# Kernel optimization log

Hardware: AMD Instinct MI355X
Metric: run time of the kernel (lower is better)

Reference implementation:

```python
import jax, jax.numpy as jnp
import numpy as np

H = 16          # num_attention_heads
DH = 64         # attention_head_size = hidden // heads
WINDOW = 128    # window_size
GLOBAL_RATIO = 0.1
SCALE = 1.0 / np.sqrt(DH)


def _combined_mask(seq_len):
    # sliding window: |i-j| <= window_size // 2
    pos = jnp.arange(seq_len)
    dist = pos[None, :] - pos[:, None]
    window_mask = jnp.abs(dist) <= (WINDOW // 2)
    # global tokens: first max(1, int(S * ratio)) positions, full row+col
    num_global = max(1, int(seq_len * GLOBAL_RATIO))
    is_global = pos < num_global
    global_mask = is_global[:, None] | is_global[None, :]
    return window_mask | global_mask  # [S, S] bool


def setup_inputs() -> dict:
    key = jax.random.key(0)
    ks = jax.random.split(key, 9)
    B, S, Dm = 2, 2048, 1024
    s = 0.02
    return {
        "hidden_states": jax.random.normal(ks[0], (B, S, Dm), jnp.float32),
        "Wq": jax.random.normal(ks[1], (Dm, Dm), jnp.float32) * s,
        "bq": jax.random.normal(ks[2], (Dm,), jnp.float32) * s,
        "Wk": jax.random.normal(ks[3], (Dm, Dm), jnp.float32) * s,
        "bk": jax.random.normal(ks[4], (Dm,), jnp.float32) * s,
        "Wv": jax.random.normal(ks[5], (Dm, Dm), jnp.float32) * s,
        "bv": jax.random.normal(ks[6], (Dm,), jnp.float32) * s,
        "Wo": jax.random.normal(ks[7], (Dm, Dm), jnp.float32) * s,
        "bo": jax.random.normal(ks[8], (Dm,), jnp.float32) * s,
    }


def reference(hidden_states, Wq, bq, Wk, bk, Wv, bv, Wo, bo):
    B, S, Dm = hidden_states.shape

    def heads(x):  # [B,S,Dm] -> [B,H,S,Dh]
        return x.reshape(B, S, H, DH).transpose(0, 2, 1, 3)

    q = heads(hidden_states @ Wq.T + bq)
    k = heads(hidden_states @ Wk.T + bk)
    v = heads(hidden_states @ Wv.T + bv)

    scores = jnp.einsum("bhqd,bhkd->bhqk", q, k) * SCALE
    mask = _combined_mask(S)  # [S,S] bool, True = attend
    scores = scores + jnp.where(mask, 0.0, -10000.0)[None, None]

    probs = jax.nn.softmax(scores, axis=-1)
    ctx = jnp.einsum("bhqk,bhkd->bhqd", probs, v)
    ctx = ctx.transpose(0, 2, 1, 3).reshape(B, S, Dm)
    return ctx @ Wo.T + bo
```

## Files before the change

### kernel.cpp

```cpp
#include <hip/hip_runtime.h>


#define B_   2
#define S_   2048
#define DM   1024
#define H_   16
#define NG   204
#define BS_  4096
#define SCL2 0.1803368801111204f
#define NEGF -3.0e38f

typedef unsigned short u16;
typedef unsigned int   u32;
typedef __attribute__((ext_vector_type(8))) short frag8;
typedef __attribute__((ext_vector_type(4))) short frag4;
typedef __attribute__((ext_vector_type(4))) float f32x4;

#define MFMA16(A, Bf, C) __builtin_amdgcn_mfma_f32_16x16x32_bf16((A), (Bf), (C), 0, 0, 0)

__device__ __forceinline__ f32x4 mfma_16x16x16_bf16(frag4 a, frag4 b, f32x4 c) {
#if defined(__HIP_DEVICE_COMPILE__)
  return __builtin_amdgcn_mfma_f32_16x16x16bf16_1k(a, b, c, 0, 0, 0);
#else
  (void)a; (void)b;
  return c;
#endif
}

#define GLD16(g, l)                                                              \
  __builtin_amdgcn_global_load_lds((const __attribute__((address_space(1))) u32*)(g), \
                                   (__attribute__((address_space(3))) u32*)(l), 16, 0, 0)
#define EXP2(x) exp2f(x)

__device__ __forceinline__ u16 f2bf(float f) {
  union { float f; u32 u; } c; c.f = f;
  u32 u = c.u + 0x7fffu + ((c.u >> 16) & 1u);
  return (u16)(u >> 16);
}

#if defined(__HIP_DEVICE_COMPILE__)
__device__ __forceinline__ u32 cvtpk_bf16(float lo, float hi) {
  u32 r;
  asm("v_cvt_pk_bf16_f32 %0, %1, %2" : "=v"(r) : "v"(lo), "v"(hi));
  return r;
}
#else
__device__ __forceinline__ u32 cvtpk_bf16(float lo, float hi) { (void)lo; (void)hi; return 0; }
#endif

__device__ __forceinline__ frag4 pack4_bf16(float a, float b, float c, float d) {
  union { u32 u[2]; frag4 f; } x;
  x.u[0] = cvtpk_bf16(a, b);
  x.u[1] = cvtpk_bf16(c, d);
  return x.f;
}

__global__ void cvt_all(const float* __restrict__ X,  const float* __restrict__ Wq,
                        const float* __restrict__ Wk, const float* __restrict__ Wv,
                        const float* __restrict__ Wo,
                        u16* Xb, u16* Wqb, u16* Wkb, u16* Wvb, u16* Wob) {
  const int chunk = blockIdx.y;
  const float* src; u16* dst;
  if (chunk < 4)      { src = X + (size_t)chunk * 1048576; dst = Xb + (size_t)chunk * 1048576; }
  else if (chunk == 4){ src = Wq; dst = Wqb; }
  else if (chunk == 5){ src = Wk; dst = Wkb; }
  else if (chunk == 6){ src = Wv; dst = Wvb; }
  else                { src = Wo; dst = Wob; }
  int i = blockIdx.x * 256 + threadIdx.x;
  float4 v = ((const float4*)src)[i];
  u32 lo = (u32)f2bf(v.x) | ((u32)f2bf(v.y) << 16);
  u32 hi = (u32)f2bf(v.z) | ((u32)f2bf(v.w) << 16);
  ((uint2*)dst)[i] = make_uint2(lo, hi);
}

__device__ __forceinline__ void gemm_mainloop(const u16* __restrict__ A, const u16* __restrict__ Bm,
                                              int bm, int bn, u16* As, u16* Bs,
                                              f32x4 acc[4][4]) {
  const int tid = threadIdx.x;
  const int wv = tid >> 6, lane = tid & 63, l15 = lane & 15, quad = lane >> 4;
  const int wm = wv & 1, wn = wv >> 1;

  const u16* gA[4]; const u16* gB[4];
#pragma unroll
  for (int c = 0; c < 4; ++c) {
    int idx = (wv * 4 + c) * 64 + lane;
    int r = idx >> 3;
    int cb = (idx & 7) ^ (r & 7);
    gA[c] = A  + (size_t)(bm + r) * DM + cb * 8;
    gB[c] = Bm + (size_t)(bn + r) * DM + cb * 8;
  }

  int offA[4][2], offB[4][2];
#pragma unroll
  for (int i = 0; i < 4; ++i)
#pragma unroll
    for (int h = 0; h < 2; ++h) {
      int mA = wm * 64 + i * 16 + l15;
      int mB = wn * 64 + i * 16 + l15;
      int cb = (quad + h * 4) ^ (l15 & 7);
      offA[i][h] = ((mA << 3) + cb) << 4;
      offB[i][h] = ((mB << 3) + cb) << 4;
    }

  for (int k0 = 0; k0 < DM; k0 += 64) {
#pragma unroll
    for (int c = 0; c < 4; ++c) {
      GLD16(gA[c] + k0, (char*)As + (wv * 4 + c) * 1024);
      GLD16(gB[c] + k0, (char*)Bs + (wv * 4 + c) * 1024);
    }
    __syncthreads();
    frag8 af[4][2], bf[4][2];
#pragma unroll
    for (int i = 0; i < 4; ++i) {
      af[i][0] = *(const frag8*)((const char*)As + offA[i][0]);
      af[i][1] = *(const frag8*)((const char*)As + offA[i][1]);
      bf[i][0] = *(const frag8*)((const char*)Bs + offB[i][0]);
      bf[i][1] = *(const frag8*)((const char*)Bs + offB[i][1]);
    }
#pragma unroll
    for (int h = 0; h < 2; ++h)
#pragma unroll
      for (int i = 0; i < 4; ++i)
#pragma unroll
        for (int j = 0; j < 4; ++j)
          acc[i][j] = MFMA16(af[i][h], bf[j][h], acc[i][j]);
    __syncthreads();
  }
}

__global__ __launch_bounds__(256, 3) void gemm_qkv(const u16* __restrict__ Xb,
    const u16* __restrict__ Wqb, const u16* __restrict__ Wkb, const u16* __restrict__ Wvb,
    const float* __restrict__ bq, const float* __restrict__ bk, const float* __restrict__ bv,
    u16* __restrict__ Qb, u16* __restrict__ Kb, u16* __restrict__ Vt) {
  __shared__ u16 As[8192], Bs[8192];
  const int bm = blockIdx.y * 128;
  const int which = blockIdx.x >> 3;
  const int bnl = (blockIdx.x & 7) * 128;
  const u16* W = (which == 0) ? Wqb : (which == 1) ? Wkb : Wvb;
  const float* bias = (which == 0) ? bq : (which == 1) ? bk : bv;

  f32x4 acc[4][4] = {};
  gemm_mainloop(Xb, W, bm, bnl, As, Bs, acc);

  const int tid = threadIdx.x, wv = tid >> 6, lane = tid & 63, l15 = lane & 15, quad = lane >> 4;
  const int wm = wv & 1, wn = wv >> 1;
  if (which < 2) {
    u16* O = (which == 0) ? Qb : Kb;
    const float scl = (which == 0) ? SCL2 : 1.0f;
#pragma unroll
    for (int j = 0; j < 4; ++j) {
      int col = bnl + wn * 64 + j * 16 + l15;
      float bb = bias[col];
#pragma unroll
      for (int i = 0; i < 4; ++i) {
        int row0 = bm + wm * 64 + i * 16 + quad * 4;
#pragma unroll
        for (int r = 0; r < 4; ++r)
          O[(size_t)(row0 + r) * DM + col] = f2bf((acc[i][j][r] + bb) * scl);
      }
    }
  } else {
#pragma unroll
    for (int j = 0; j < 4; ++j) {
      int col = bnl + wn * 64 + j * 16 + l15;
      float bb = bias[col];
#pragma unroll
      for (int i = 0; i < 4; ++i) {
        int row0 = bm + wm * 64 + i * 16 + quad * 4;
        u32 lo = (u32)f2bf(acc[i][j][0] + bb) | ((u32)f2bf(acc[i][j][1] + bb) << 16);
        u32 hi = (u32)f2bf(acc[i][j][2] + bb) | ((u32)f2bf(acc[i][j][3] + bb) << 16);
        *(uint2*)&Vt[(size_t)col * BS_ + row0] = make_uint2(lo, hi);
      }
    }
  }
}

__global__ __launch_bounds__(256, 3) void gemm_wo(const u16* __restrict__ Cx,
    const u16* __restrict__ Wob, const float* __restrict__ bo, float* __restrict__ out) {
  __shared__ u16 As[8192], Bs[8192];
  const int bm = blockIdx.y * 128, bn = blockIdx.x * 128;

  f32x4 acc[4][4] = {};
  gemm_mainloop(Cx, Wob, bm, bn, As, Bs, acc);

  const int tid = threadIdx.x, wv = tid >> 6, lane = tid & 63, l15 = lane & 15, quad = lane >> 4;
  const int wm = wv & 1, wn = wv >> 1;
#pragma unroll
  for (int j = 0; j < 4; ++j) {
    int col = bn + wn * 64 + j * 16 + l15;
    float bb = bo[col];
#pragma unroll
    for (int i = 0; i < 4; ++i) {
      int row0 = bm + wm * 64 + i * 16 + quad * 4;
#pragma unroll
      for (int r = 0; r < 4; ++r)
        out[(size_t)(row0 + r) * DM + col] = acc[i][j][r] + bb;
    }
  }
}

__global__ __launch_bounds__(256, 3) void attn_kernel(const u16* __restrict__ Q,
                                                      const u16* __restrict__ K,
                                                      const u16* __restrict__ Vt,
                                                      u16* __restrict__ Ctx,
                                                      float* __restrict__ Op,
                                                      float* __restrict__ Lp) {
  __shared__ u16 Ks[2][4096];
  __shared__ u16 Vs[2][4096];

  const int tid = threadIdx.x, w = tid >> 6, lane = tid & 63, l15 = lane & 15, quad = lane >> 4;
  const int blk = blockIdx.x;
  const int bh = blk & 31, unit = blk >> 5;
  const int b = bh >> 4, h = bh & 15;
  const bool heavy = unit < 8;
  const int strip = heavy ? (unit >> 2) : 0;
  const int q0 = heavy ? strip * 128 : 256 + (unit - 8) * 128;
  const int qw = q0 + w * 16;

  frag8 bq[2][2];
#pragma unroll
  for (int g = 0; g < 2; ++g) {
    const u16* qrow = Q + (size_t)(b * S_ + qw + g * 64 + l15) * DM + h * 64;
    bq[g][0] = *(const frag8*)(qrow + quad * 8);
    bq[g][1] = *(const frag8*)(qrow + quad * 8 + 32);
  }

  const u16* gK[2]; const u16* gV[2]; int ldso[2];
#pragma unroll
  for (int c = 0; c < 2; ++c) {
    int sl = (w * 2 + c) * 64 + lane;
    int r = sl >> 3;
    int fr = (r & 7) ^ (((r >> 3) & 1) << 2);
    int cb = (sl & 7) ^ fr;
    gK[c] = K  + (size_t)(b * S_ + r) * DM + h * 64 + cb * 8;
    gV[c] = Vt + (size_t)(h * 64 + r) * BS_ + (size_t)b * S_ + cb * 8;
    ldso[c] = (w * 2 + c) * 1024;
  }

  const int fl = (l15 & 7) ^ (((l15 >> 3) & 1) << 2);
  int offKb[2];
#pragma unroll
  for (int hh = 0; hh < 2; ++hh)
    offKb[hh] = ((l15 << 3) + ((quad + hh * 4) ^ fl)) << 4;
  int offVb[4];
#pragma unroll
  for (int kg = 0; kg < 4; ++kg)
    offVb[kg] = ((((l15 << 3) + ((((kg << 1) | (quad >> 1))) ^ fl)) << 4)
                 | ((quad & 1) << 3));

  int mlo[2]; u32 mspan[2];
#pragma unroll
  for (int g = 0; g < 2; ++g) {
    int qi = qw + g * 64 + l15;
    bool qg = qi < NG;
    mlo[g]   = qg ? (int)0x80000000 : (qi - 64);
    mspan[g] = qg ? 0xFFFFFFFFu : 128u;
  }
  const frag4 ones = {(short)0x3F80, (short)0x3F80, (short)0x3F80, (short)0x3F80};

  f32x4 o[2][4] = {};
  f32x4 o_l[2] = {};

  auto stage = [&](int t, int buf) {
#pragma unroll
    for (int c = 0; c < 2; ++c) {
      GLD16(gK[c] + (size_t)t * 64 * DM, (char*)Ks[buf] + ldso[c]);
      GLD16(gV[c] + t * 64,              (char*)Vs[buf] + ldso[c]);
    }
  };

  auto step = [&](int kt, int p, int mmode) {
    int gok0 = 1, gok1 = 1;
    if (mmode == 1) {
      const int k0s = kt * 64;
      const int ql1 = qw + 64;
      gok0 = (qw  < NG) || ((k0s + 63 >= qw  - 64) && (k0s <= qw  + 79));
      gok1 = (ql1 < NG) || ((k0s + 63 >= ql1 - 64) && (k0s <= ql1 + 79));
      if (!(gok0 | gok1)) return;
    }
    const char* kb_ = (const char*)Ks[p];
    const char* vb_ = (const char*)Vs[p];
    frag8 ak[4][2];
#pragma unroll
    for (int kg = 0; kg < 4; ++kg) {
      ak[kg][0] = *(const frag8*)(kb_ + offKb[0] + kg * 2048);
      ak[kg][1] = *(const frag8*)(kb_ + offKb[1] + kg * 2048);
    }
    const int k0 = kt * 64;
    const int gok[2] = {gok0, gok1};
    frag4 pk[2][4];
#pragma unroll
    for (int g = 0; g < 2; ++g) {
      if (!gok[g]) continue;
      f32x4 st[4] = {};
#pragma unroll
      for (int kg = 0; kg < 4; ++kg) {
        st[kg] = MFMA16(ak[kg][0], bq[g][0], st[kg]);
        st[kg] = MFMA16(ak[kg][1], bq[g][1], st[kg]);
      }
      if (mmode) {
#pragma unroll
        for (int kg = 0; kg < 4; ++kg) {
          float pr[4];
#pragma unroll
          for (int r = 0; r < 4; ++r) {
            int kc = k0 + kg * 16 + quad * 4 + r;
            bool act = ((u32)(kc - mlo[g]) <= mspan[g]);
            if (mmode == 2) act = act || (kc < NG);
            float e = EXP2(st[kg][r]);
            pr[r] = act ? e : 0.0f;
          }
          pk[g][kg] = pack4_bf16(pr[0], pr[1], pr[2], pr[3]);
        }
      } else {
#pragma unroll
        for (int kg = 0; kg < 4; ++kg)
          pk[g][kg] = pack4_bf16(EXP2(st[kg][0]), EXP2(st[kg][1]),
                                 EXP2(st[kg][2]), EXP2(st[kg][3]));
      }
    }
    if (gok0 & gok1) {
#pragma unroll
      for (int kg = 0; kg < 4; ++kg) {
        o_l[0] = mfma_16x16x16_bf16(ones, pk[0][kg], o_l[0]);
        o_l[1] = mfma_16x16x16_bf16(ones, pk[1][kg], o_l[1]);
#pragma unroll
        for (int nt = 0; nt < 4; ++nt) {
          frag4 av = *(const frag4*)(vb_ + offVb[kg] + nt * 2048);
          o[0][nt] = mfma_16x16x16_bf16(av, pk[0][kg], o[0][nt]);
          o[1][nt] = mfma_16x16x16_bf16(av, pk[1][kg], o[1][nt]);
        }
      }
    } else if (gok0) {
#pragma unroll
      for (int kg = 0; kg < 4; ++kg) {
        o_l[0] = mfma_16x16x16_bf16(ones, pk[0][kg], o_l[0]);
#pragma unroll
        for (int nt = 0; nt < 4; ++nt) {
          frag4 av = *(const frag4*)(vb_ + offVb[kg] + nt * 2048);
          o[0][nt] = mfma_16x16x16_bf16(av, pk[0][kg], o[0][nt]);
        }
      }
    } else {
#pragma unroll
      for (int kg = 0; kg < 4; ++kg) {
        o_l[1] = mfma_16x16x16_bf16(ones, pk[1][kg], o_l[1]);
#pragma unroll
        for (int nt = 0; nt < 4; ++nt) {
          frag4 av = *(const frag4*)(vb_ + offVb[kg] + nt * 2048);
          o[1][nt] = mfma_16x16x16_bf16(av, pk[1][kg], o[1][nt]);
        }
      }
    }
  };

  if (heavy) {
    const int seg = unit & 3;
    const int kt0 = seg * 8;
    const bool dm = (strip == 1);
    int p = 0;
    stage(kt0, 0);
#pragma unroll 1
    for (int tt = 0; tt < 8; ++tt) {
      __syncthreads();
      if (tt < 7) stage(kt0 + tt + 1, p ^ 1);
      const int kt = kt0 + tt;
      const int mm = dm ? ((kt == 3) ? 2 : ((kt > 2) ? 1 : 0)) : 0;
      step(kt, p, mm);
      p ^= 1;
    }
    float* op = Op + ((size_t)((bh * 2 + strip) * 4 + seg)) * 8192;
    float* lp = Lp + ((size_t)((bh * 2 + strip) * 4 + seg)) * 128;
#pragma unroll
    for (int g = 0; g < 2; ++g) {
      int rl = g * 64 + w * 16 + l15;
      if (quad == 0) lp[rl] = o_l[g][0];
#pragma unroll
      for (int nt = 0; nt < 4; ++nt)
        *(float4*)&op[rl * 64 + nt * 16 + quad * 4] =
            make_float4(o[g][nt][0], o[g][nt][1], o[g][nt][2], o[g][nt][3]);
    }
    return;
  }

  auto activef = [&](int t) {
    int k0 = t * 64;
    return (k0 < NG) || (k0 + 63 >= q0 - 64 && k0 <= q0 + 127 + 64);
  };
  auto nextt = [&](int cur) { int n = cur + 1; while (n < 32 && !activef(n)) ++n; return n; };

  int kt = 0, p = 0;
  stage(0, 0);
  for (;;) {
    int ktn = nextt(kt);
    bool more = ktn < 32;
    __syncthreads();
    if (more) stage(ktn, p ^ 1);
    const int mm = (kt == 3) ? 2 : ((kt > 2) ? 1 : 0);
    step(kt, p, mm);
    if (!more) break;
    kt = ktn; p ^= 1;
  }

#pragma unroll
  for (int g = 0; g < 2; ++g) {
    float inv = 1.0f / o_l[g][0];
    u16* crow = Ctx + (size_t)((size_t)b * S_ + qw + g * 64 + l15) * DM + h * 64;
#pragma unroll
    for (int nt = 0; nt < 4; ++nt) {
      u32 lo = (u32)f2bf(o[g][nt][0] * inv) | ((u32)f2bf(o[g][nt][1] * inv) << 16);
      u32 hi = (u32)f2bf(o[g][nt][2] * inv) | ((u32)f2bf(o[g][nt][3] * inv) << 16);
      *(uint2*)&crow[nt * 16 + quad * 4] = make_uint2(lo, hi);
    }
  }
}

__global__ __launch_bounds__(256) void combine_kernel(const float* __restrict__ Op,
                                                      const float* __restrict__ Lp,
                                                      u16* __restrict__ Ctx) {
  const int blk = blockIdx.x;
  const int bh = blk & 31, s64 = blk >> 5;
  const int b = bh >> 4, h = bh & 15;
  const int t = threadIdx.x;
  const int row = t >> 2, colg = (t & 3) * 16;
  const int gq = s64 * 64 + row;
  const int strip = gq >> 7, rIn = gq & 127;

  const float* opb = Op + ((size_t)(bh * 2 + strip) * 4) * 8192;
  const float* lpb = Lp + ((size_t)(bh * 2 + strip) * 4) * 128;

  float l = lpb[rIn] + lpb[128 + rIn] + lpb[256 + rIn] + lpb[384 + rIn];
  float acc[16];
#pragma unroll
  for (int e = 0; e < 16; ++e) acc[e] = opb[rIn * 64 + colg + e];
#pragma unroll
  for (int seg = 1; seg < 4; ++seg)
#pragma unroll
    for (int e = 0; e < 16; ++e) acc[e] += opb[seg * 8192 + rIn * 64 + colg + e];

  float inv = 1.0f / l;
  u32 pk[8];
#pragma unroll
  for (int p = 0; p < 8; ++p)
    pk[p] = (u32)f2bf(acc[2 * p] * inv) | ((u32)f2bf(acc[2 * p + 1] * inv) << 16);
  u16* dst = Ctx + (size_t)((size_t)b * S_ + gq) * DM + h * 64 + colg;
  *(uint4*)dst       = make_uint4(pk[0], pk[1], pk[2], pk[3]);
  *(uint4*)(dst + 8) = make_uint4(pk[4], pk[5], pk[6], pk[7]);
}

extern "C" void kernel_launch(void* const* d_in, const int* in_sizes, int n_in,
                              void* d_out, int out_size, void* d_ws, size_t ws_size,
                              hipStream_t stream) {
  const float* X  = (const float*)d_in[0];
  const float* Wq = (const float*)d_in[1];
  const float* bq = (const float*)d_in[2];
  const float* Wk = (const float*)d_in[3];
  const float* bk = (const float*)d_in[4];
  const float* Wv = (const float*)d_in[5];
  const float* bv = (const float*)d_in[6];
  const float* Wo = (const float*)d_in[7];
  const float* bo = (const float*)d_in[8];
  float* out = (float*)d_out;

  u16* ws = (u16*)d_ws;
  const size_t NX = (size_t)BS_ * DM;
  const size_t NW = (size_t)DM * DM;
  u16* Xb  = ws;
  u16* Wqb = Xb + NX;
  u16* Wkb = Wqb + NW;
  u16* Wvb = Wkb + NW;
  u16* Wob = Wvb + NW;
  u16* Qb  = Wob + NW;
  u16* Kb  = Qb + NX;
  u16* Vt  = Kb + NX;
  u16* Cx  = Vt + NX;
  float* Op = (float*)(Cx + NX);
  float* Lp = Op + (size_t)32 * 2 * 4 * 8192;

  cvt_all<<<dim3(1024, 8), 256, 0, stream>>>(X, Wq, Wk, Wv, Wo, Xb, Wqb, Wkb, Wvb, Wob);
  gemm_qkv<<<dim3(24, 32), 256, 0, stream>>>(Xb, Wqb, Wkb, Wvb, bq, bk, bv, Qb, Kb, Vt);
  attn_kernel<<<22 * 32, 256, 0, stream>>>(Qb, Kb, Vt, Cx, Op, Lp);
  combine_kernel<<<128, 256, 0, stream>>>(Op, Lp, Cx);
  gemm_wo<<<dim3(8, 32), 256, 0, stream>>>(Cx, Wob, bo, out);
}
```

Measured before the change: 173.6 us.

## Fuse split-K combine into attention via atomic counters; skip masked 16-key subtiles

Removes the separate combine kernel launch: each heavy attention block atomically increments a per-strip counter, and the last of the four segment blocks reduces the partial O and L buffers and writes the bf16 context. Counters are zeroed inside the conversion kernel. The masked step now computes a per-16-key-group activity mask for each query group and skips K fragment loads, QK MFMAs, exp and PV MFMAs for fully masked groups. The cost is atomics, fences and a serialized tail reduction in one block, plus more branching in the inner loop.

```diff
diff --git a/kernel.cpp b/kernel.cpp
--- a/kernel.cpp
+++ b/kernel.cpp
@@ -58,8 +58,10 @@
 __global__ void cvt_all(const float* __restrict__ X,  const float* __restrict__ Wq,
                         const float* __restrict__ Wk, const float* __restrict__ Wv,
                         const float* __restrict__ Wo,
-                        u16* Xb, u16* Wqb, u16* Wkb, u16* Wvb, u16* Wob) {
+                        u16* Xb, u16* Wqb, u16* Wkb, u16* Wvb, u16* Wob,
+                        u32* cnt) {
   const int chunk = blockIdx.y;
+  if (chunk == 0 && blockIdx.x == 0 && threadIdx.x < 64) cnt[threadIdx.x] = 0;
   const float* src; u16* dst;
   if (chunk < 4)      { src = X + (size_t)chunk * 1048576; dst = Xb + (size_t)chunk * 1048576; }
   else if (chunk == 4){ src = Wq; dst = Wqb; }
@@ -204,9 +206,11 @@
                                                       const u16* __restrict__ Vt,
                                                       u16* __restrict__ Ctx,
                                                       float* __restrict__ Op,
-                                                      float* __restrict__ Lp) {
+                                                      float* __restrict__ Lp,
+                                                      u32* __restrict__ Cnt) {
   __shared__ u16 Ks[2][4096];
   __shared__ u16 Vs[2][4096];
+  __shared__ u32 sOld;
 
   const int tid = threadIdx.x, w = tid >> 6, lane = tid & 63, l15 = lane & 15, quad = lane >> 4;
   const int blk = blockIdx.x;
@@ -270,86 +274,103 @@
   };
 
   auto step = [&](int kt, int p, int mmode) {
-    int gok0 = 1, gok1 = 1;
-    if (mmode == 1) {
-      const int k0s = kt * 64;
-      const int ql1 = qw + 64;
-      gok0 = (qw  < NG) || ((k0s + 63 >= qw  - 64) && (k0s <= qw  + 79));
-      gok1 = (ql1 < NG) || ((k0s + 63 >= ql1 - 64) && (k0s <= ql1 + 79));
-      if (!(gok0 | gok1)) return;
-    }
+    const int k0 = kt * 64;
+    unsigned m0 = 0xFu, m1 = 0xFu;
+    if (mmode) {
+      m0 = 0u; m1 = 0u;
+      const int qlo0 = qw, qlo1 = qw + 64;
+      const bool ag0 = qlo0 < NG, ag1 = qlo1 < NG;
+#pragma unroll
+      for (int kg = 0; kg < 4; ++kg) {
+        const int klo = k0 + kg * 16, khi = klo + 15;
+        const bool cg = (mmode == 2) && (klo < NG);
+        if (ag0 | cg | ((khi >= qlo0 - 64) & (klo <= qlo0 + 79))) m0 |= 1u << kg;
+        if (ag1 | cg | ((khi >= qlo1 - 64) & (klo <= qlo1 + 79))) m1 |= 1u << kg;
+      }
+      if (!(m0 | m1)) return;
+    }
+    const unsigned mu = m0 | m1;
     const char* kb_ = (const char*)Ks[p];
     const char* vb_ = (const char*)Vs[p];
     frag8 ak[4][2];
 #pragma unroll
-    for (int kg = 0; kg < 4; ++kg) {
-      ak[kg][0] = *(const frag8*)(kb_ + offKb[0] + kg * 2048);
-      ak[kg][1] = *(const frag8*)(kb_ + offKb[1] + kg * 2048);
-    }
-    const int k0 = kt * 64;
-    const int gok[2] = {gok0, gok1};
+    for (int kg = 0; kg < 4; ++kg)
+      if ((mu >> kg) & 1) {
+        ak[kg][0] = *(const frag8*)(kb_ + offKb[0] + kg * 2048);
+        ak[kg][1] = *(const frag8*)(kb_ + offKb[1] + kg * 2048);
+      }
     frag4 pk[2][4];
-#pragma unroll
-    for (int g = 0; g < 2; ++g) {
-      if (!gok[g]) continue;
+    if (m0) {
       f32x4 st[4] = {};
 #pragma unroll
-      for (int kg = 0; kg < 4; ++kg) {
-        st[kg] = MFMA16(ak[kg][0], bq[g][0], st[kg]);
-        st[kg] = MFMA16(ak[kg][1], bq[g][1], st[kg]);
-      }
+      for (int kg = 0; kg < 4; ++kg)
+        if ((m0 >> kg) & 1) {
+          st[kg] = MFMA16(ak[kg][0], bq[0][0], st[kg]);
+          st[kg] = MFMA16(ak[kg][1], bq[0][1], st[kg]);
+        }
       if (mmode) {
 #pragma unroll
         for (int kg = 0; kg < 4; ++kg) {
+          if (!((m0 >> kg) & 1)) continue;
           float pr[4];
 #pragma unroll
           for (int r = 0; r < 4; ++r) {
             int kc = k0 + kg * 16 + quad * 4 + r;
-            bool act = ((u32)(kc - mlo[g]) <= mspan[g]);
+            bool act = ((u32)(kc - mlo[0]) <= mspan[0]);
             if (mmode == 2) act = act || (kc < NG);
             float e = EXP2(st[kg][r]);
             pr[r] = act ? e : 0.0f;
           }
-          pk[g][kg] = pack4_bf16(pr[0], pr[1], pr[2], pr[3]);
+          pk[0][kg] = pack4_bf16(pr[0], pr[1], pr[2], pr[3]);
         }
       } else {
 #pragma unroll
         for (int kg = 0; kg < 4; ++kg)
-          pk[g][kg] = pack4_bf16(EXP2(st[kg][0]), EXP2(st[kg][1]),
+          pk[0][kg] = pack4_bf16(EXP2(st[kg][0]), EXP2(st[kg][1]),
                                  EXP2(st[kg][2]), EXP2(st[kg][3]));
       }
     }
-    if (gok0 & gok1) {
-#pragma unroll
-      for (int kg = 0; kg < 4; ++kg) {
-        o_l[0] = mfma_16x16x16_bf16(ones, pk[0][kg], o_l[0]);
-        o_l[1] = mfma_16x16x16_bf16(ones, pk[1][kg], o_l[1]);
-#pragma unroll
-        for (int nt = 0; nt < 4; ++nt) {
-          frag4 av = *(const frag4*)(vb_ + offVb[kg] + nt * 2048);
-          o[0][nt] = mfma_16x16x16_bf16(av, pk[0][kg], o[0][nt]);
-          o[1][nt] = mfma_16x16x16_bf16(av, pk[1][kg], o[1][nt]);
+    if (m1) {
+      f32x4 st[4] = {};
+#pragma unroll
+      for (int kg = 0; kg < 4; ++kg)
+        if ((m1 >> kg) & 1) {
+          st[kg] = MFMA16(ak[kg][0], bq[1][0], st[kg]);
+          st[kg] = MFMA16(ak[kg][1], bq[1][1], st[kg]);
         }
-      }
-    } else if (gok0) {
-#pragma unroll
-      for (int kg = 0; kg < 4; ++kg) {
-        o_l[0] = mfma_16x16x16_bf16(ones, pk[0][kg], o_l[0]);
-#pragma unroll
-        for (int nt = 0; nt < 4; ++nt) {
-          frag4 av = *(const frag4*)(vb_ + offVb[kg] + nt * 2048);
-          o[0][nt] = mfma_16x16x16_bf16(av, pk[0][kg], o[0][nt]);
+      if (mmode) {
+#pragma unroll
+        for (int kg = 0; kg < 4; ++kg) {
+          if (!((m1 >> kg) & 1)) continue;
+          float pr[4];
+#pragma unroll
+          for (int r = 0; r < 4; ++r) {
+            int kc = k0 + kg * 16 + quad * 4 + r;
+            bool act = ((u32)(kc - mlo[1]) <= mspan[1]);
+            if (mmode == 2) act = act || (kc < NG);
+            float e = EXP2(st[kg][r]);
+            pr[r] = act ? e : 0.0f;
+          }
+          pk[1][kg] = pack4_bf16(pr[0], pr[1], pr[2], pr[3]);
         }
-      }
-    } else {
-#pragma unroll
-      for (int kg = 0; kg < 4; ++kg) {
-        o_l[1] = mfma_16x16x16_bf16(ones, pk[1][kg], o_l[1]);
-#pragma unroll
-        for (int nt = 0; nt < 4; ++nt) {
-          frag4 av = *(const frag4*)(vb_ + offVb[kg] + nt * 2048);
-          o[1][nt] = mfma_16x16x16_bf16(av, pk[1][kg], o[1][nt]);
-        }
+      } else {
+#pragma unroll
+        for (int kg = 0; kg < 4; ++kg)
+          pk[1][kg] = pack4_bf16(EXP2(st[kg][0]), EXP2(st[kg][1]),
+                                 EXP2(st[kg][2]), EXP2(st[kg][3]));
+      }
+    }
+#pragma unroll
+    for (int kg = 0; kg < 4; ++kg) {
+      const bool a0 = (m0 >> kg) & 1, a1 = (m1 >> kg) & 1;
+      if (!(a0 | a1)) continue;
+      if (a0) o_l[0] = mfma_16x16x16_bf16(ones, pk[0][kg], o_l[0]);
+      if (a1) o_l[1] = mfma_16x16x16_bf16(ones, pk[1][kg], o_l[1]);
+#pragma unroll
+      for (int nt = 0; nt < 4; ++nt) {
+        frag4 av = *(const frag4*)(vb_ + offVb[kg] + nt * 2048);
+        if (a0) o[0][nt] = mfma_16x16x16_bf16(av, pk[0][kg], o[0][nt]);
+        if (a1) o[1][nt] = mfma_16x16x16_bf16(av, pk[1][kg], o[1][nt]);
       }
     }
   };
@@ -380,6 +401,43 @@
         *(float4*)&op[rl * 64 + nt * 16 + quad * 4] =
             make_float4(o[g][nt][0], o[g][nt][1], o[g][nt][2], o[g][nt][3]);
     }
+    __syncthreads();
+    if (tid == 0) {
+      __threadfence();
+      sOld = atomicAdd(&Cnt[bh * 2 + strip], 1u);
+    }
+    __syncthreads();
+    if (sOld == 3u) {
+      __threadfence();
+      const int rIn = tid >> 1, colg = (tid & 1) * 32;
+      const float* opb = Op + (size_t)((bh * 2 + strip) * 4) * 8192;
+      const float* lpb = Lp + (size_t)((bh * 2 + strip) * 4) * 128;
+      float l = 0.0f;
+#pragma unroll
+      for (int s = 0; s < 4; ++s)
+        l += __hip_atomic_load(lpb + s * 128 + rIn, __ATOMIC_RELAXED,
+                               __HIP_MEMORY_SCOPE_AGENT);
+      float accv[32];
+#pragma unroll
+      for (int e = 0; e < 32; ++e) accv[e] = 0.0f;
+#pragma unroll
+      for (int s = 0; s < 4; ++s)
+#pragma unroll
+        for (int e = 0; e < 32; ++e)
+          accv[e] += __hip_atomic_load(opb + s * 8192 + rIn * 64 + colg + e,
+                                       __ATOMIC_RELAXED, __HIP_MEMORY_SCOPE_AGENT);
+      const float inv = 1.0f / l;
+      const int gq = strip * 128 + rIn;
+      u16* dst = Ctx + (size_t)((size_t)b * S_ + gq) * DM + h * 64 + colg;
+      u32 pw[16];
+#pragma unroll
+      for (int e = 0; e < 16; ++e)
+        pw[e] = (u32)f2bf(accv[2 * e] * inv) | ((u32)f2bf(accv[2 * e + 1] * inv) << 16);
+#pragma unroll
+      for (int q4 = 0; q4 < 4; ++q4)
+        *(uint4*)(dst + q4 * 8) = make_uint4(pw[4 * q4], pw[4 * q4 + 1],
+                                             pw[4 * q4 + 2], pw[4 * q4 + 3]);
+    }
     return;
   }
 
@@ -413,39 +471,6 @@
       *(uint2*)&crow[nt * 16 + quad * 4] = make_uint2(lo, hi);
     }
   }
-}
-
-__global__ __launch_bounds__(256) void combine_kernel(const float* __restrict__ Op,
-                                                      const float* __restrict__ Lp,
-                                                      u16* __restrict__ Ctx) {
-  const int blk = blockIdx.x;
-  const int bh = blk & 31, s64 = blk >> 5;
-  const int b = bh >> 4, h = bh & 15;
-  const int t = threadIdx.x;
-  const int row = t >> 2, colg = (t & 3) * 16;
-  const int gq = s64 * 64 + row;
-  const int strip = gq >> 7, rIn = gq & 127;
-
-  const float* opb = Op + ((size_t)(bh * 2 + strip) * 4) * 8192;
-  const float* lpb = Lp + ((size_t)(bh * 2 + strip) * 4) * 128;
-
-  float l = lpb[rIn] + lpb[128 + rIn] + lpb[256 + rIn] + lpb[384 + rIn];
-  float acc[16];
-#pragma unroll
-  for (int e = 0; e < 16; ++e) acc[e] = opb[rIn * 64 + colg + e];
-#pragma unroll
-  for (int seg = 1; seg < 4; ++seg)
-#pragma unroll
-    for (int e = 0; e < 16; ++e) acc[e] += opb[seg * 8192 + rIn * 64 + colg + e];
-
-  float inv = 1.0f / l;
-  u32 pk[8];
-#pragma unroll
-  for (int p = 0; p < 8; ++p)
-    pk[p] = (u32)f2bf(acc[2 * p] * inv) | ((u32)f2bf(acc[2 * p + 1] * inv) << 16);
-  u16* dst = Ctx + (size_t)((size_t)b * S_ + gq) * DM + h * 64 + colg;
-  *(uint4*)dst       = make_uint4(pk[0], pk[1], pk[2], pk[3]);
-  *(uint4*)(dst + 8) = make_uint4(pk[4], pk[5], pk[6], pk[7]);
 }
 
 extern "C" void kernel_launch(void* const* d_in, const int* in_sizes, int n_in,
@@ -476,10 +501,10 @@
   u16* Cx  = Vt + NX;
   float* Op = (float*)(Cx + NX);
   float* Lp = Op + (size_t)32 * 2 * 4 * 8192;
-
-  cvt_all<<<dim3(1024, 8), 256, 0, stream>>>(X, Wq, Wk, Wv, Wo, Xb, Wqb, Wkb, Wvb, Wob);
+  u32*   Cnt = (u32*)(Lp + (size_t)32 * 2 * 4 * 128);
+
+  cvt_all<<<dim3(1024, 8), 256, 0, stream>>>(X, Wq, Wk, Wv, Wo, Xb, Wqb, Wkb, Wvb, Wob, Cnt);
   gemm_qkv<<<dim3(24, 32), 256, 0, stream>>>(Xb, Wqb, Wkb, Wvb, bq, bk, bv, Qb, Kb, Vt);
-  attn_kernel<<<22 * 32, 256, 0, stream>>>(Qb, Kb, Vt, Cx, Op, Lp);
-  combine_kernel<<<128, 256, 0, stream>>>(Op, Lp, Cx);
+  attn_kernel<<<22 * 32, 256, 0, stream>>>(Qb, Kb, Vt, Cx, Op, Lp, Cnt);
   gemm_wo<<<dim3(8, 32), 256, 0, stream>>>(Cx, Wob, bo, out);
 }
```

Result: slower. 207.2 us (+19.4%).

## Fuse split-K combine into attention kernel via last-block atomic counter

Applied to the files above, without the earlier changes.

Removes the separate combine kernel launch. Each heavy attention block now increments a per-(bh,strip) counter after writing its partial output. The fourth block to arrive sums the four partial O/L slices and writes the normalized bf16 context. The counter is zeroed inside the conversion kernel, which saves one launch and its gap at the cost of fences, atomics and a serialized tail inside the last block.

```diff
diff --git a/kernel.cpp b/kernel.cpp
--- a/kernel.cpp
+++ b/kernel.cpp
@@ -58,8 +58,10 @@
 __global__ void cvt_all(const float* __restrict__ X,  const float* __restrict__ Wq,
                         const float* __restrict__ Wk, const float* __restrict__ Wv,
                         const float* __restrict__ Wo,
-                        u16* Xb, u16* Wqb, u16* Wkb, u16* Wvb, u16* Wob) {
+                        u16* Xb, u16* Wqb, u16* Wkb, u16* Wvb, u16* Wob,
+                        u32* cnt) {
   const int chunk = blockIdx.y;
+  if (chunk == 0 && blockIdx.x == 0 && threadIdx.x < 64) cnt[threadIdx.x] = 0;
   const float* src; u16* dst;
   if (chunk < 4)      { src = X + (size_t)chunk * 1048576; dst = Xb + (size_t)chunk * 1048576; }
   else if (chunk == 4){ src = Wq; dst = Wqb; }
@@ -204,9 +206,11 @@
                                                       const u16* __restrict__ Vt,
                                                       u16* __restrict__ Ctx,
                                                       float* __restrict__ Op,
-                                                      float* __restrict__ Lp) {
+                                                      float* __restrict__ Lp,
+                                                      u32* __restrict__ Cnt) {
   __shared__ u16 Ks[2][4096];
   __shared__ u16 Vs[2][4096];
+  __shared__ u32 sOld;
 
   const int tid = threadIdx.x, w = tid >> 6, lane = tid & 63, l15 = lane & 15, quad = lane >> 4;
   const int blk = blockIdx.x;
@@ -380,6 +384,43 @@
         *(float4*)&op[rl * 64 + nt * 16 + quad * 4] =
             make_float4(o[g][nt][0], o[g][nt][1], o[g][nt][2], o[g][nt][3]);
     }
+    __syncthreads();
+    if (tid == 0) {
+      __threadfence();
+      sOld = atomicAdd(&Cnt[bh * 2 + strip], 1u);
+    }
+    __syncthreads();
+    if (sOld == 3u) {
+      __threadfence();
+      const int rIn = tid >> 1, colg = (tid & 1) * 32;
+      const float* opb = Op + (size_t)((bh * 2 + strip) * 4) * 8192;
+      const float* lpb = Lp + (size_t)((bh * 2 + strip) * 4) * 128;
+      float l = 0.0f;
+#pragma unroll
+      for (int s = 0; s < 4; ++s)
+        l += __hip_atomic_load(lpb + s * 128 + rIn, __ATOMIC_RELAXED,
+                               __HIP_MEMORY_SCOPE_AGENT);
+      float accv[32];
+#pragma unroll
+      for (int e = 0; e < 32; ++e) accv[e] = 0.0f;
+#pragma unroll
+      for (int s = 0; s < 4; ++s)
+#pragma unroll
+        for (int e = 0; e < 32; ++e)
+          accv[e] += __hip_atomic_load(opb + s * 8192 + rIn * 64 + colg + e,
+                                       __ATOMIC_RELAXED, __HIP_MEMORY_SCOPE_AGENT);
+      const float inv = 1.0f / l;
+      const int gq = strip * 128 + rIn;
+      u16* dst = Ctx + (size_t)((size_t)b * S_ + gq) * DM + h * 64 + colg;
+      u32 pw[16];
+#pragma unroll
+      for (int e = 0; e < 16; ++e)
+        pw[e] = (u32)f2bf(accv[2 * e] * inv) | ((u32)f2bf(accv[2 * e + 1] * inv) << 16);
+#pragma unroll
+      for (int q4 = 0; q4 < 4; ++q4)
+        *(uint4*)(dst + q4 * 8) = make_uint4(pw[4 * q4], pw[4 * q4 + 1],
+                                             pw[4 * q4 + 2], pw[4 * q4 + 3]);
+    }
     return;
   }
 
@@ -413,39 +454,6 @@
       *(uint2*)&crow[nt * 16 + quad * 4] = make_uint2(lo, hi);
     }
   }
-}
-
-__global__ __launch_bounds__(256) void combine_kernel(const float* __restrict__ Op,
-                                                      const float* __restrict__ Lp,
-                                                      u16* __restrict__ Ctx) {
-  const int blk = blockIdx.x;
-  const int bh = blk & 31, s64 = blk >> 5;
-  const int b = bh >> 4, h = bh & 15;
-  const int t = threadIdx.x;
-  const int row = t >> 2, colg = (t & 3) * 16;
-  const int gq = s64 * 64 + row;
-  const int strip = gq >> 7, rIn = gq & 127;
-
-  const float* opb = Op + ((size_t)(bh * 2 + strip) * 4) * 8192;
-  const float* lpb = Lp + ((size_t)(bh * 2 + strip) * 4) * 128;
-
-  float l = lpb[rIn] + lpb[128 + rIn] + lpb[256 + rIn] + lpb[384 + rIn];
-  float acc[16];
-#pragma unroll
-  for (int e = 0; e < 16; ++e) acc[e] = opb[rIn * 64 + colg + e];
-#pragma unroll
-  for (int seg = 1; seg < 4; ++seg)
-#pragma unroll
-    for (int e = 0; e < 16; ++e) acc[e] += opb[seg * 8192 + rIn * 64 + colg + e];
-
-  float inv = 1.0f / l;
-  u32 pk[8];
-#pragma unroll
-  for (int p = 0; p < 8; ++p)
-    pk[p] = (u32)f2bf(acc[2 * p] * inv) | ((u32)f2bf(acc[2 * p + 1] * inv) << 16);
-  u16* dst = Ctx + (size_t)((size_t)b * S_ + gq) * DM + h * 64 + colg;
-  *(uint4*)dst       = make_uint4(pk[0], pk[1], pk[2], pk[3]);
-  *(uint4*)(dst + 8) = make_uint4(pk[4], pk[5], pk[6], pk[7]);
 }
 
 extern "C" void kernel_launch(void* const* d_in, const int* in_sizes, int n_in,
@@ -476,10 +484,10 @@
   u16* Cx  = Vt + NX;
   float* Op = (float*)(Cx + NX);
   float* Lp = Op + (size_t)32 * 2 * 4 * 8192;
-
-  cvt_all<<<dim3(1024, 8), 256, 0, stream>>>(X, Wq, Wk, Wv, Wo, Xb, Wqb, Wkb, Wvb, Wob);
+  u32*   Cnt = (u32*)(Lp + (size_t)32 * 2 * 4 * 128);
+
+  cvt_all<<<dim3(1024, 8), 256, 0, stream>>>(X, Wq, Wk, Wv, Wo, Xb, Wqb, Wkb, Wvb, Wob, Cnt);
   gemm_qkv<<<dim3(24, 32), 256, 0, stream>>>(Xb, Wqb, Wkb, Wvb, bq, bk, bv, Qb, Kb, Vt);
-  attn_kernel<<<22 * 32, 256, 0, stream>>>(Qb, Kb, Vt, Cx, Op, Lp);
-  combine_kernel<<<128, 256, 0, stream>>>(Op, Lp, Cx);
+  attn_kernel<<<22 * 32, 256, 0, stream>>>(Qb, Kb, Vt, Cx, Op, Lp, Cnt);
   gemm_wo<<<dim3(8, 32), 256, 0, stream>>>(Cx, Wob, bo, out);
 }
```

Result: slower. 204.9 us (+18.0%).
